# Optimization experiments

Hardware: AMD Instinct MI355X
Metric: run time of the kernel (lower is better)

The kernel has to match this reference:

```python
import jax, jax.numpy as jnp
import numpy as np

B, N, D, F = 32, 4096, 256, 256

def setup_inputs() -> dict:
    key = jax.random.key(0)
    k1, k2, k3, k4 = jax.random.split(key, 4)
    raw_input = jax.random.normal(k1, (B, N, D), dtype=jnp.float32)
    input_plus_attention = jax.random.normal(k2, (B, F), dtype=jnp.float32)
    W = jax.random.normal(k3, (F, N), dtype=jnp.float32) * 0.02
    b = jnp.zeros((N,), dtype=jnp.float32)
    # keras 'uniform' initializer: U(-0.05, 0.05)
    threshold = jax.random.uniform(k4, (1,), minval=-0.05, maxval=0.05, dtype=jnp.float32)
    return {"raw_input": raw_input, "input_plus_attention": input_plus_attention,
            "W": W, "b": b, "threshold": threshold}

def reference(raw_input, input_plus_attention, W, b, threshold):
    # Dense(units, relu): [B,F] @ [F,N] -> [B,N]
    x = jax.nn.relu(input_plus_attention @ W + b)
    # BinaryLayer: 1.0 where x > threshold else 0.0 -> row selection mask [B,N]
    mask = x > threshold[0]
    # TF boolean_mask + reshape(B,-1,D) performs per-batch stream compaction of
    # selected rows. JAX needs static shapes, so compact selected rows to the
    # front (stable order preserved) and zero-pad the tail to length N.
    order = jnp.argsort(jnp.where(mask, 0, 1).astype(jnp.int32), axis=1)  # stable: selected first
    gathered = jnp.take_along_axis(raw_input, order[:, :, None], axis=1)  # [B,N,D]
    counts = jnp.sum(mask, axis=1, keepdims=True)                          # [B,1]
    keep = jnp.arange(N)[None, :] < counts                                 # [B,N]
    out = jnp.where(keep[:, :, None], gathered, jnp.zeros((), raw_input.dtype))
    return out
```

## Files before the change

kernel.cpp:

```cpp
#include <hip/hip_runtime.h>
#include <hip/hip_bf16.h>
#include <stdint.h>


#define BB 32
#define NN 4096
#define DD 256
#define FF 256
#define COLS 16

__global__ __launch_bounds__(256) void mask_kernel(
    const float* __restrict__ A,
    const float* __restrict__ W,
    const float* __restrict__ bias,
    const float* __restrict__ thr_p,
    uint8_t* __restrict__ mask)
{
    __shared__ float a_sh[BB * FF];
    __shared__ float w_sh[FF * COLS];

    const int t  = threadIdx.x;
    const int n0 = blockIdx.x * COLS;

    for (int i = t; i < BB * FF; i += 256) a_sh[i] = A[i];
    for (int i = t; i < FF * COLS; i += 256) {
        int f = i / COLS, c = i % COLS;
        w_sh[i] = W[(size_t)f * NN + n0 + c];
    }
    __syncthreads();

    const float thr = thr_p[0];

    for (int p = t; p < BB * COLS; p += 256) {
        const int b = p / COLS, c = p % COLS;
        const float* ap = a_sh + b * FF;
        const float* wp = w_sh + c;
        double acc0 = 0.0, acc1 = 0.0, acc2 = 0.0, acc3 = 0.0;
        #pragma unroll 4
        for (int f = 0; f < FF; f += 4) {
            acc0 += (double)ap[f + 0] * (double)wp[(f + 0) * COLS];
            acc1 += (double)ap[f + 1] * (double)wp[(f + 1) * COLS];
            acc2 += (double)ap[f + 2] * (double)wp[(f + 2) * COLS];
            acc3 += (double)ap[f + 3] * (double)wp[(f + 3) * COLS];
        }
        float v = (float)((acc0 + acc1) + (acc2 + acc3)) + bias[n0 + c];
        mask[(size_t)b * NN + n0 + c] = (fmaxf(v, 0.f) > thr) ? 1 : 0;
    }
}

__global__ __launch_bounds__(1024) void scan_kernel(
    const uint8_t* __restrict__ mask,
    int* __restrict__ order,
    int* __restrict__ count)
{
    const int b   = blockIdx.x;
    const int tid = threadIdx.x;
    __shared__ int wsum[16];

    const uchar4 m4 = reinterpret_cast<const uchar4*>(mask + (size_t)b * NN)[tid];
    const int m0 = m4.x, m1 = m4.y, m2 = m4.z, m3 = m4.w;
    const int s  = m0 + m1 + m2 + m3;
    const int n0 = tid * 4;

    const int lane = tid & 63;
    const int wid  = tid >> 6;
    int incl = s;
    #pragma unroll
    for (int d = 1; d < 64; d <<= 1) {
        int t = __shfl_up(incl, d, 64);
        if (lane >= d) incl += t;
    }
    if (lane == 63) wsum[wid] = incl;
    __syncthreads();
    if (tid == 0) {
        int run = 0;
        #pragma unroll
        for (int i = 0; i < 16; ++i) { int t = wsum[i]; wsum[i] = run; run += t; }
        count[b] = run;
    }
    __syncthreads();

    int base = wsum[wid] + (incl - s);
    int* ob = order + (size_t)b * NN;
    if (m0) ob[base++] = n0;
    if (m1) ob[base++] = n0 + 1;
    if (m2) ob[base++] = n0 + 2;
    if (m3) ob[base++] = n0 + 3;
}

__global__ __launch_bounds__(256) void gather_kernel(
    const float* __restrict__ raw,
    const int* __restrict__ order,
    const int* __restrict__ count,
    float* __restrict__ out)
{
    const int b    = blockIdx.y;
    const int wid  = threadIdx.x >> 6;
    const int lane = threadIdx.x & 63;
    const int j    = blockIdx.x * 4 + wid;

    const int cnt = count[b];
    float4* dst = reinterpret_cast<float4*>(out + ((size_t)b * NN + j) * DD) + lane;
    if (j < cnt) {
        const int src = order[(size_t)b * NN + j];
        const float4* sp =
            reinterpret_cast<const float4*>(raw + ((size_t)b * NN + src) * DD) + lane;
        *dst = *sp;
    } else {
        *dst = make_float4(0.f, 0.f, 0.f, 0.f);
    }
}

extern "C" void kernel_launch(void* const* d_in, const int* in_sizes, int n_in,
                              void* d_out, int out_size, void* d_ws, size_t ws_size,
                              hipStream_t stream) {
    const float* raw  = (const float*)d_in[0];
    const float* A    = (const float*)d_in[1];
    const float* W    = (const float*)d_in[2];
    const float* bias = (const float*)d_in[3];
    const float* thr  = (const float*)d_in[4];
    float* out = (float*)d_out;

    uint8_t* mask  = (uint8_t*)d_ws;
    int*     order = (int*)((char*)d_ws + (size_t)BB * NN);
    int*     count = order + (size_t)BB * NN;

    mask_kernel<<<NN / COLS, 256, 0, stream>>>(A, W, bias, thr, mask);
    scan_kernel<<<BB, 1024, 0, stream>>>(mask, order, count);
    gather_kernel<<<dim3(NN / 4, BB), 256, 0, stream>>>(raw, order, count, out);
}
```

Baseline: 62.20 us.

## Bit-pack mask, transpose W in LDS, and widen gather with nontemporal access

The mask kernel now stores A and a transposed W tile in padded LDS, reads them as float4 vectors, gives each thread two batch rows, and packs the mask results into 16-bit words using wave ballots. The scan kernel works on these bitmasks with popcount and bit iteration, using 256 threads per batch instead of 1024. The gather kernel copies two rows per wave and uses nontemporal loads and stores to avoid polluting the cache. Together these aim to reduce LDS bank conflicts, mask traffic and launch overhead, though the gather, which moves 128 MB, still dominates the runtime.

```diff
diff --git a/kernel.cpp b/kernel.cpp
--- a/kernel.cpp
+++ b/kernel.cpp
@@ -8,84 +8,111 @@
 #define DD 256
 #define FF 256
 #define COLS 16
+#define CH (NN / COLS)
+#define ASTRIDE (FF + 4)
+
+typedef float f4 __attribute__((ext_vector_type(4)));
 
 __global__ __launch_bounds__(256) void mask_kernel(
     const float* __restrict__ A,
     const float* __restrict__ W,
     const float* __restrict__ bias,
     const float* __restrict__ thr_p,
-    uint8_t* __restrict__ mask)
+    uint16_t* __restrict__ bits)
 {
-    __shared__ float a_sh[BB * FF];
-    __shared__ float w_sh[FF * COLS];
+    __shared__ float a_sh[BB * ASTRIDE];
+    __shared__ float wT[COLS * ASTRIDE];
 
-    const int t  = threadIdx.x;
-    const int n0 = blockIdx.x * COLS;
+    const int t     = threadIdx.x;
+    const int chunk = blockIdx.x;
+    const int n0    = chunk * COLS;
 
-    for (int i = t; i < BB * FF; i += 256) a_sh[i] = A[i];
+    for (int i = t; i < BB * FF; i += 256) {
+        int b = i >> 8, f = i & 255;
+        a_sh[b * ASTRIDE + f] = A[i];
+    }
     for (int i = t; i < FF * COLS; i += 256) {
-        int f = i / COLS, c = i % COLS;
-        w_sh[i] = W[(size_t)f * NN + n0 + c];
+        int f = i >> 4, c = i & 15;
+        wT[c * ASTRIDE + f] = W[(size_t)f * NN + n0 + c];
     }
     __syncthreads();
 
     const float thr = thr_p[0];
+    const int c  = t & 15;
+    const int b1 = t >> 4;
+    const int b2 = b1 + 16;
 
-    for (int p = t; p < BB * COLS; p += 256) {
-        const int b = p / COLS, c = p % COLS;
-        const float* ap = a_sh + b * FF;
-        const float* wp = w_sh + c;
-        double acc0 = 0.0, acc1 = 0.0, acc2 = 0.0, acc3 = 0.0;
-        #pragma unroll 4
-        for (int f = 0; f < FF; f += 4) {
-            acc0 += (double)ap[f + 0] * (double)wp[(f + 0) * COLS];
-            acc1 += (double)ap[f + 1] * (double)wp[(f + 1) * COLS];
-            acc2 += (double)ap[f + 2] * (double)wp[(f + 2) * COLS];
-            acc3 += (double)ap[f + 3] * (double)wp[(f + 3) * COLS];
-        }
-        float v = (float)((acc0 + acc1) + (acc2 + acc3)) + bias[n0 + c];
-        mask[(size_t)b * NN + n0 + c] = (fmaxf(v, 0.f) > thr) ? 1 : 0;
+    const f4* a1p = reinterpret_cast<const f4*>(a_sh + b1 * ASTRIDE);
+    const f4* a2p = reinterpret_cast<const f4*>(a_sh + b2 * ASTRIDE);
+    const f4* wp  = reinterpret_cast<const f4*>(wT   + c  * ASTRIDE);
+
+    double s0 = 0.0, s1 = 0.0, s2 = 0.0, s3 = 0.0;
+    #pragma unroll 8
+    for (int fs = 0; fs < FF / 4; ++fs) {
+        f4 w4 = wp[fs];
+        f4 a1 = a1p[fs];
+        f4 a2 = a2p[fs];
+        s0 = fma((double)a1.x, (double)w4.x, s0);
+        s0 = fma((double)a1.y, (double)w4.y, s0);
+        s1 = fma((double)a1.z, (double)w4.z, s1);
+        s1 = fma((double)a1.w, (double)w4.w, s1);
+        s2 = fma((double)a2.x, (double)w4.x, s2);
+        s2 = fma((double)a2.y, (double)w4.y, s2);
+        s3 = fma((double)a2.z, (double)w4.z, s3);
+        s3 = fma((double)a2.w, (double)w4.w, s3);
+    }
+    const float bi = bias[n0 + c];
+    const float v1 = (float)(s0 + s1) + bi;
+    const float v2 = (float)(s2 + s3) + bi;
+    const int m1 = (fmaxf(v1, 0.f) > thr) ? 1 : 0;
+    const int m2 = (fmaxf(v2, 0.f) > thr) ? 1 : 0;
+
+    unsigned long long bal1 = __ballot(m1);
+    unsigned long long bal2 = __ballot(m2);
+    if (c == 0) {
+        const int g = (t & 63) >> 4;
+        bits[b1 * CH + chunk] = (uint16_t)((bal1 >> (16 * g)) & 0xFFFF);
+        bits[b2 * CH + chunk] = (uint16_t)((bal2 >> (16 * g)) & 0xFFFF);
     }
 }
 
-__global__ __launch_bounds__(1024) void scan_kernel(
-    const uint8_t* __restrict__ mask,
+__global__ __launch_bounds__(256) void scan_kernel(
+    const uint16_t* __restrict__ bits,
     int* __restrict__ order,
     int* __restrict__ count)
 {
-    const int b   = blockIdx.x;
-    const int tid = threadIdx.x;
-    __shared__ int wsum[16];
+    const int b = blockIdx.x;
+    const int t = threadIdx.x;
+    __shared__ int wsum[4];
 
-    const uchar4 m4 = reinterpret_cast<const uchar4*>(mask + (size_t)b * NN)[tid];
-    const int m0 = m4.x, m1 = m4.y, m2 = m4.z, m3 = m4.w;
-    const int s  = m0 + m1 + m2 + m3;
-    const int n0 = tid * 4;
+    unsigned m = bits[b * CH + t];
+    const int s = __popc(m);
 
-    const int lane = tid & 63;
-    const int wid  = tid >> 6;
+    const int lane = t & 63;
+    const int wid  = t >> 6;
     int incl = s;
     #pragma unroll
     for (int d = 1; d < 64; d <<= 1) {
-        int t = __shfl_up(incl, d, 64);
-        if (lane >= d) incl += t;
+        int x = __shfl_up(incl, d, 64);
+        if (lane >= d) incl += x;
     }
     if (lane == 63) wsum[wid] = incl;
     __syncthreads();
-    if (tid == 0) {
+    if (t == 0) {
         int run = 0;
         #pragma unroll
-        for (int i = 0; i < 16; ++i) { int t = wsum[i]; wsum[i] = run; run += t; }
+        for (int i = 0; i < 4; ++i) { int x = wsum[i]; wsum[i] = run; run += x; }
         count[b] = run;
     }
     __syncthreads();
 
     int base = wsum[wid] + (incl - s);
-    int* ob = order + (size_t)b * NN;
-    if (m0) ob[base++] = n0;
-    if (m1) ob[base++] = n0 + 1;
-    if (m2) ob[base++] = n0 + 2;
-    if (m3) ob[base++] = n0 + 3;
+    int* ob = order + (size_t)b * NN + base;
+    const int n0 = t * COLS;
+    while (m) {
+        *ob++ = n0 + (__ffs(m) - 1);
+        m &= m - 1;
+    }
 }
 
 __global__ __launch_bounds__(256) void gather_kernel(
@@ -97,18 +124,25 @@
     const int b    = blockIdx.y;
     const int wid  = threadIdx.x >> 6;
     const int lane = threadIdx.x & 63;
-    const int j    = blockIdx.x * 4 + wid;
+    const int j0   = blockIdx.x * 8 + wid * 2;
 
     const int cnt = count[b];
-    float4* dst = reinterpret_cast<float4*>(out + ((size_t)b * NN + j) * DD) + lane;
-    if (j < cnt) {
-        const int src = order[(size_t)b * NN + j];
-        const float4* sp =
-            reinterpret_cast<const float4*>(raw + ((size_t)b * NN + src) * DD) + lane;
-        *dst = *sp;
-    } else {
-        *dst = make_float4(0.f, 0.f, 0.f, 0.f);
+    const int* ob = order + (size_t)b * NN;
+    const f4* rawp = reinterpret_cast<const f4*>(raw);
+    f4* outp = reinterpret_cast<f4*>(out);
+
+    f4 r0 = {0.f, 0.f, 0.f, 0.f};
+    f4 r1 = {0.f, 0.f, 0.f, 0.f};
+    if (j0 < cnt) {
+        const int src = ob[j0];
+        r0 = __builtin_nontemporal_load(rawp + ((size_t)b * NN + src) * (DD / 4) + lane);
     }
+    if (j0 + 1 < cnt) {
+        const int src = ob[j0 + 1];
+        r1 = __builtin_nontemporal_load(rawp + ((size_t)b * NN + src) * (DD / 4) + lane);
+    }
+    __builtin_nontemporal_store(r0, outp + ((size_t)b * NN + j0)     * (DD / 4) + lane);
+    __builtin_nontemporal_store(r1, outp + ((size_t)b * NN + j0 + 1) * (DD / 4) + lane);
 }
 
 extern "C" void kernel_launch(void* const* d_in, const int* in_sizes, int n_in,
@@ -121,11 +155,11 @@
     const float* thr  = (const float*)d_in[4];
     float* out = (float*)d_out;
 
-    uint8_t* mask  = (uint8_t*)d_ws;
-    int*     order = (int*)((char*)d_ws + (size_t)BB * NN);
-    int*     count = order + (size_t)BB * NN;
+    uint16_t* bits  = (uint16_t*)d_ws;
+    int*      order = (int*)((char*)d_ws + 65536);
+    int*      count = order + (size_t)BB * NN;
 
-    mask_kernel<<<NN / COLS, 256, 0, stream>>>(A, W, bias, thr, mask);
-    scan_kernel<<<BB, 1024, 0, stream>>>(mask, order, count);
-    gather_kernel<<<dim3(NN / 4, BB), 256, 0, stream>>>(raw, order, count, out);
+    mask_kernel<<<CH, 256, 0, stream>>>(A, W, bias, thr, bits);
+    scan_kernel<<<BB, 256, 0, stream>>>(bits, order, count);
+    gather_kernel<<<dim3(NN / 8, BB), 256, 0, stream>>>(raw, order, count, out);
 }
```

New measurement: 60.08 us. 3.4% less time.
